# Kernel optimization log

Hardware: AMD Instinct MI355X
Metric: run time of the kernel (lower is better)

Reference implementation:

```python
import jax, jax.numpy as jnp
import numpy as np

B, CIN, N = 4, 128, 4096
CKEY, COUT = 64, 128

def setup_inputs() -> dict:
    key = jax.random.key(0)
    k1, k2, k3, k4 = jax.random.split(key, 4)
    x = jax.random.normal(k1, (B, CIN, N), dtype=jnp.float32)
    # Conv1d(kernel_size=1, bias=False) weights as [out, in] matrices
    Wq = jax.random.normal(k2, (CKEY, CIN), dtype=jnp.float32) * (1.0 / np.sqrt(CIN))
    Wk = jax.random.normal(k3, (CKEY, CIN), dtype=jnp.float32) * (1.0 / np.sqrt(CIN))
    Wv = jax.random.normal(k4, (COUT, CIN), dtype=jnp.float32) * (1.0 / np.sqrt(CIN))
    return {"x": x, "Wq": Wq, "Wk": Wk, "Wv": Wv}

def reference(x, Wq, Wk, Wv):
    # 1x1 conv projections: [B, C, N] -> [B, C', N]
    Q = jnp.einsum('ki,bin->bkn', Wq, x)   # [B, CKEY, N]
    K = jnp.einsum('ki,bin->bkn', Wk, x)   # [B, CKEY, N]
    V = jnp.einsum('oi,bin->bon', Wv, x)   # [B, COUT, N]
    # A = softmax(Q^T K) over last dim -- NOTE: no 1/sqrt(d) scaling, as in original
    scores = jnp.einsum('bkn,bkm->bnm', Q, K)     # [B, N, N]
    A = jax.nn.softmax(scores, axis=2)
    # out = (A @ V^T)^T -> [B, COUT, N]
    out = jnp.einsum('bnm,bom->bon', A, V)
    return out
```

## Files before the change

### kernel.cpp

```cpp
#include <hip/hip_runtime.h>
#include <hip/hip_bf16.h>

#define NN    4096
#define BB    4
#define CIN_  128
#define CKEY_ 64
#define COUT_ 128

typedef __attribute__((ext_vector_type(8))) short bf16x8;
typedef __attribute__((ext_vector_type(4))) short bf16x4;
typedef __attribute__((ext_vector_type(4))) float f32x4;

#define MFMA16 __builtin_amdgcn_mfma_f32_16x16x32_bf16
#define SWK(row, c) ((((row) << 6)) + ((((c) ^ ((row) & 7))) << 3))

__device__ __forceinline__ float bf2f(short s) {
    union { unsigned int u; float f; } c; c.u = ((unsigned int)(unsigned short)s) << 16; return c.f;
}
__device__ __forceinline__ short f2bf(float f) {
    union { float f; unsigned int u; } c; c.f = f;
    unsigned int r = c.u + 0x7fffu + ((c.u >> 16) & 1u);
    return (short)(r >> 16);
}
__device__ __forceinline__ float fexp2(float x) {
#if __has_builtin(__builtin_amdgcn_exp2f)
    return __builtin_amdgcn_exp2f(x);
#else
    return exp2f(x);
#endif
}
__device__ __forceinline__ unsigned int pack_bf16(float a, float b) {
    union { float f; unsigned int u; } ca, cb; ca.f = a; cb.f = b;
    unsigned int ua = ca.u + 0x8000u, ub = cb.u + 0x8000u;
#if __has_builtin(__builtin_amdgcn_perm)
    return __builtin_amdgcn_perm(ub, ua, 0x07060302u);
#else
    return (ua >> 16) | (ub & 0xffff0000u);
#endif
}

__global__ __launch_bounds__(256) void wcvt_kernel(const float* __restrict__ Wq,
                                                   const float* __restrict__ Wk,
                                                   const float* __restrict__ Wv,
                                                   short* __restrict__ Whf,
                                                   short* __restrict__ Wlf) {
    int id   = blockIdx.x * 256 + threadIdx.x;
    int l15  = id & 15;
    int quad = (id >> 4) & 3;
    int kc   = (id >> 6) & 3;
    int g    = id >> 8;
    int out  = g * 16 + l15;
    int k0   = kc * 32 + quad * 8;

    const float* src;
    float scale = 1.0f;
    if (out < 64)       { src = Wq + out * CIN_;         scale = 1.4426950408889634f; }
    else if (out < 128) { src = Wk + (out - 64) * CIN_; }
    else                { src = Wv + (out - 128) * CIN_; }

    bf16x8 h8, l8;
#pragma unroll
    for (int j = 0; j < 8; ++j) {
        float w = src[k0 + j] * scale;
        short h = f2bf(w);
        h8[j] = h;
        l8[j] = f2bf(w - bf2f(h));
    }
    *(bf16x8*)(Whf + id * 8) = h8;
    *(bf16x8*)(Wlf + id * 8) = l8;
}

__global__ __launch_bounds__(256) void proj_kernel(const float* __restrict__ x,
                                                   const short* __restrict__ Whf,
                                                   const short* __restrict__ Wlf,
                                                   short* __restrict__ Qh, short* __restrict__ Ql,
                                                   short* __restrict__ Kh, short* __restrict__ Kl,
                                                   short* __restrict__ Vb) {
    __shared__ __align__(16) short xsh[16 * 64 * 8];
    __shared__ __align__(16) short xsl[16 * 64 * 8];

    int tid  = threadIdx.x;
    int b    = blockIdx.y;
    int gz   = blockIdx.z;
    int gn0  = blockIdx.x * 64;
    int wave = tid >> 6;
    int lane = tid & 63;
    int quad = lane >> 4;
    int l15  = lane & 15;

    const float* xb = x + (size_t)b * CIN_ * NN + gn0;
#pragma unroll
    for (int rep = 0; rep < 4; ++rep) {
        int slot = rep * 256 + tid;
        int c = slot >> 6, n = slot & 63;
        bf16x8 h8, l8;
#pragma unroll
        for (int j = 0; j < 8; ++j) {
            float f = xb[(c * 8 + j) * NN + n];
            short h = f2bf(f);
            h8[j] = h;
            l8[j] = f2bf(f - bf2f(h));
        }
        *(bf16x8*)(xsh + (c * 64 + n) * 8) = h8;
        *(bf16x8*)(xsl + (c * 64 + n) * 8) = l8;
    }
    __syncthreads();

#pragma unroll
    for (int rr = 0; rr < 2; ++rr) {
        int rg = gz * 8 + rr * 4 + wave;
        f32x4 acc[4];
#pragma unroll
        for (int ct = 0; ct < 4; ++ct) acc[ct] = (f32x4){0.f, 0.f, 0.f, 0.f};

#pragma unroll
        for (int kc = 0; kc < 4; ++kc) {
            bf16x8 wh = *(const bf16x8*)(Whf + ((((rg * 4 + kc) * 4 + quad) * 16) + l15) * 8);
            bf16x8 wl = *(const bf16x8*)(Wlf + ((((rg * 4 + kc) * 4 + quad) * 16) + l15) * 8);
#pragma unroll
            for (int ct = 0; ct < 4; ++ct) {
                bf16x8 xh = *(const bf16x8*)(xsh + (((kc * 4 + quad) * 64) + ct * 16 + l15) * 8);
                bf16x8 xl = *(const bf16x8*)(xsl + (((kc * 4 + quad) * 64) + ct * 16 + l15) * 8);
                acc[ct] = MFMA16(wh, xh, acc[ct], 0, 0, 0);
                acc[ct] = MFMA16(wh, xl, acc[ct], 0, 0, 0);
                acc[ct] = MFMA16(wl, xh, acc[ct], 0, 0, 0);
            }
        }

        if (rg < 8) {
            short* H = (rg < 4) ? Qh : Kh;
            short* L = (rg < 4) ? Ql : Kl;
            int rb    = (rg < 4) ? rg : (rg - 4);
            int chunk = rb * 2 + (quad >> 1);
            int sub   = (quad & 1) * 4;
#pragma unroll
            for (int ct = 0; ct < 4; ++ct) {
                int n = gn0 + ct * 16 + l15;
                bf16x4 h4, l4;
#pragma unroll
                for (int r = 0; r < 4; ++r) {
                    float f = acc[ct][r];
                    short h = f2bf(f);
                    h4[r] = h;
                    l4[r] = f2bf(f - bf2f(h));
                }
                *(bf16x4*)(H + (((b * 8 + chunk) * NN) + n) * 8 + sub) = h4;
                *(bf16x4*)(L + (((b * 8 + chunk) * NN) + n) * 8 + sub) = l4;
            }
        } else {
            int o0 = rg * 16 + quad * 4 - 128;
#pragma unroll
            for (int ct = 0; ct < 4; ++ct) {
                int n = gn0 + ct * 16 + l15;
#pragma unroll
                for (int r = 0; r < 4; ++r)
                    Vb[((size_t)(b * COUT_ + o0 + r)) * NN + n] = f2bf(acc[ct][r]);
            }
        }
    }
}

__global__ __launch_bounds__(256, 2) void flash_kernel(const short* __restrict__ Qh,
                                                       const short* __restrict__ Ql,
                                                       const short* __restrict__ Kh,
                                                       const short* __restrict__ Kl,
                                                       const short* __restrict__ Vb,
                                                       float* __restrict__ outp,
                                                       float* __restrict__ ml,
                                                       int S, int direct) {
    __shared__ __align__(16) short KhT[64 * 64];
    __shared__ __align__(16) short KlT[64 * 64];
    __shared__ __align__(16) short VT[128 * 64];

    int tid  = threadIdx.x;
    int bx   = blockIdx.x;
    int b    = bx / S;
    int s    = bx - b * S;
    int qt   = blockIdx.y;
    int wave = tid >> 6;
    int lane = tid & 63;
    int quad = lane >> 4;
    int l15  = lane & 15;

    int nq0 = qt * 128 + wave * 32 + l15;
    bf16x8 qh0[2], qh1[2], ql0[2], ql1[2];
#pragma unroll
    for (int u = 0; u < 2; ++u) {
        int nq = nq0 + u * 16;
        qh0[u] = *(const bf16x8*)(Qh + (((b * 8 + quad)     * NN) + nq) * 8);
        qh1[u] = *(const bf16x8*)(Qh + (((b * 8 + 4 + quad) * NN) + nq) * 8);
        ql0[u] = *(const bf16x8*)(Ql + (((b * 8 + quad)     * NN) + nq) * 8);
        ql1[u] = *(const bf16x8*)(Ql + (((b * 8 + 4 + quad) * NN) + nq) * 8);
    }

    f32x4 O[2][8];
#pragma unroll
    for (int u = 0; u < 2; ++u)
#pragma unroll
        for (int f = 0; f < 8; ++f) O[u][f] = (f32x4){0.f, 0.f, 0.f, 0.f};
    float m_i[2] = {-1.0e30f, -1.0e30f}, l_i[2] = {0.f, 0.f};

    int krow = tid & 63, kc2 = (tid >> 6) * 2;
    int vrow = tid & 127, vc0 = (tid >> 7) * 4;
    int sl0 = (quad & 1) * 32 + l15;
    int sl1 = sl0 + 16;
    int fsel = quad >> 1;

    int KPS   = NN / S;
    int kb    = s * KPS;
    int iters = KPS / 64;

    const short* KhB = Kh + (size_t)b * 8 * NN * 8;
    const short* KlB = Kl + (size_t)b * 8 * NN * 8;
    const short* VbB = Vb + (size_t)b * COUT_ * NN;

    bf16x8 nkh[2], nkl[2], nv[4];
#pragma unroll
    for (int cc = 0; cc < 2; ++cc) {
        int c = kc2 + cc;
        nkh[cc] = *(const bf16x8*)(KhB + ((c * NN) + kb + krow) * 8);
        nkl[cc] = *(const bf16x8*)(KlB + ((c * NN) + kb + krow) * 8);
    }
#pragma unroll
    for (int q = 0; q < 4; ++q)
        nv[q] = *(const bf16x8*)(VbB + (size_t)vrow * NN + kb + (vc0 + q) * 8);

    for (int it = 0; it < iters; ++it) {
#pragma unroll
        for (int cc = 0; cc < 2; ++cc) {
            int c = kc2 + cc;
            *(bf16x8*)(KhT + SWK(krow, c)) = nkh[cc];
            *(bf16x8*)(KlT + SWK(krow, c)) = nkl[cc];
        }
#pragma unroll
        for (int q = 0; q < 4; ++q)
            *(bf16x8*)(VT + SWK(vrow, vc0 + q)) = nv[q];
        __syncthreads();

        if (it + 1 < iters) {
            int nb = kb + 64;
#pragma unroll
            for (int cc = 0; cc < 2; ++cc) {
                int c = kc2 + cc;
                nkh[cc] = *(const bf16x8*)(KhB + ((c * NN) + nb + krow) * 8);
                nkl[cc] = *(const bf16x8*)(KlB + ((c * NN) + nb + krow) * 8);
            }
#pragma unroll
            for (int q = 0; q < 4; ++q)
                nv[q] = *(const bf16x8*)(VbB + (size_t)vrow * NN + nb + (vc0 + q) * 8);
        }

        f32x4 sA[2][4];
#pragma unroll
        for (int f = 0; f < 4; ++f) {
            int row = f * 16 + l15;
            bf16x8 kh0 = *(const bf16x8*)(KhT + SWK(row, quad));
            bf16x8 kh1 = *(const bf16x8*)(KhT + SWK(row, 4 + quad));
            bf16x8 kl0 = *(const bf16x8*)(KlT + SWK(row, quad));
            bf16x8 kl1 = *(const bf16x8*)(KlT + SWK(row, 4 + quad));
#pragma unroll
            for (int u = 0; u < 2; ++u) {
                f32x4 acc = (f32x4){0.f, 0.f, 0.f, 0.f};
                acc = MFMA16(kh0, qh0[u], acc, 0, 0, 0);
                acc = MFMA16(kh1, qh1[u], acc, 0, 0, 0);
                acc = MFMA16(kl0, qh0[u], acc, 0, 0, 0);
                acc = MFMA16(kl1, qh1[u], acc, 0, 0, 0);
                acc = MFMA16(kh0, ql0[u], acc, 0, 0, 0);
                acc = MFMA16(kh1, ql1[u], acc, 0, 0, 0);
                sA[u][f] = acc;
            }
        }

        unsigned int pw[2][4][2];
#pragma unroll
        for (int u = 0; u < 2; ++u) {
            float vm = sA[u][0][0];
#pragma unroll
            for (int f = 0; f < 4; ++f)
#pragma unroll
                for (int r = 0; r < 4; ++r) vm = fmaxf(vm, sA[u][f][r]);
            vm = fmaxf(vm, __shfl_xor(vm, 16, 64));
            vm = fmaxf(vm, __shfl_xor(vm, 32, 64));
            float nm    = fmaxf(m_i[u], vm);
            float alpha = fexp2(m_i[u] - nm);
            m_i[u] = nm;

            float p[4][4];
            float rs = 0.f;
#pragma unroll
            for (int f = 0; f < 4; ++f)
#pragma unroll
                for (int r = 0; r < 4; ++r) {
                    float pv = fexp2(sA[u][f][r] - nm);
                    p[f][r] = pv;
                    rs += pv;
                }
            rs += __shfl_xor(rs, 16, 64);
            rs += __shfl_xor(rs, 32, 64);
            l_i[u] = l_i[u] * alpha + rs;

            if (__any(alpha < 1.0f)) {
#pragma unroll
                for (int f = 0; f < 8; ++f)
#pragma unroll
                    for (int r = 0; r < 4; ++r) O[u][f][r] *= alpha;
            }
#pragma unroll
            for (int f = 0; f < 4; ++f) {
                pw[u][f][0] = pack_bf16(p[f][0], p[f][1]);
                pw[u][f][1] = pack_bf16(p[f][2], p[f][3]);
            }
        }

#pragma unroll
        for (int g = 0; g < 2; ++g) {
            union { int i[4]; bf16x8 v; } pb[2];
#pragma unroll
            for (int u = 0; u < 2; ++u) {
                int a0 = __shfl((int)pw[u][g * 2][0],     sl0, 64);
                int a1 = __shfl((int)pw[u][g * 2][1],     sl0, 64);
                int a2 = __shfl((int)pw[u][g * 2][0],     sl1, 64);
                int a3 = __shfl((int)pw[u][g * 2][1],     sl1, 64);
                int b0 = __shfl((int)pw[u][g * 2 + 1][0], sl0, 64);
                int b1 = __shfl((int)pw[u][g * 2 + 1][1], sl0, 64);
                int b2 = __shfl((int)pw[u][g * 2 + 1][0], sl1, 64);
                int b3 = __shfl((int)pw[u][g * 2 + 1][1], sl1, 64);
                pb[u].i[0] = fsel ? b0 : a0;
                pb[u].i[1] = fsel ? b1 : a1;
                pb[u].i[2] = fsel ? b2 : a2;
                pb[u].i[3] = fsel ? b3 : a3;
            }
#pragma unroll
            for (int f8 = 0; f8 < 8; ++f8) {
                bf16x8 vA = *(const bf16x8*)(VT + SWK(f8 * 16 + l15, g * 4 + quad));
                O[0][f8] = MFMA16(vA, pb[0].v, O[0][f8], 0, 0, 0);
                O[1][f8] = MFMA16(vA, pb[1].v, O[1][f8], 0, 0, 0);
            }
        }
        __syncthreads();
        kb += 64;
    }

#pragma unroll
    for (int u = 0; u < 2; ++u) {
        int n = nq0 + u * 16;
        if (direct) {
            float inv = 1.f / l_i[u];
#pragma unroll
            for (int f8 = 0; f8 < 8; ++f8)
#pragma unroll
                for (int r = 0; r < 4; ++r) {
                    int o = f8 * 16 + quad * 4 + r;
                    outp[((size_t)(b * COUT_ + o)) * NN + n] = O[u][f8][r] * inv;
                }
        } else {
#pragma unroll
            for (int f8 = 0; f8 < 8; ++f8)
#pragma unroll
                for (int r = 0; r < 4; ++r) {
                    int o = f8 * 16 + quad * 4 + r;
                    outp[((size_t)((b * S + s) * COUT_ + o)) * NN + n] = O[u][f8][r];
                }
            if (quad == 0) {
                ml[((b * S + s) * 2 + 0) * NN + n] = m_i[u];
                ml[((b * S + s) * 2 + 1) * NN + n] = l_i[u];
            }
        }
    }
}

__global__ __launch_bounds__(256, 4) void merge_kernel(const float* __restrict__ Opart,
                                                       const float* __restrict__ ml,
                                                       float* __restrict__ out, int S) {
    int idx = blockIdx.x * 256 + threadIdx.x;
    int n0  = (idx & (NN / 4 - 1)) * 4;
    int rest = idx >> 10;
    int o = rest & (COUT_ - 1);
    int b = rest >> 7;

    f32x4 gm = (f32x4){-1.0e30f, -1.0e30f, -1.0e30f, -1.0e30f};
    for (int s = 0; s < S; ++s) {
        f32x4 m = *(const f32x4*)(ml + ((b * S + s) * 2 + 0) * NN + n0);
#pragma unroll
        for (int j = 0; j < 4; ++j) gm[j] = fmaxf(gm[j], m[j]);
    }
    f32x4 acc = (f32x4){0.f, 0.f, 0.f, 0.f};
    f32x4 den = (f32x4){0.f, 0.f, 0.f, 0.f};
    for (int s = 0; s < S; ++s) {
        f32x4 m = *(const f32x4*)(ml + ((b * S + s) * 2 + 0) * NN + n0);
        f32x4 l = *(const f32x4*)(ml + ((b * S + s) * 2 + 1) * NN + n0);
        f32x4 ov = *(const f32x4*)(Opart + ((size_t)((b * S + s) * COUT_ + o)) * NN + n0);
#pragma unroll
        for (int j = 0; j < 4; ++j) {
            float ws = fexp2(m[j] - gm[j]);
            acc[j] = fmaf(ws, ov[j], acc[j]);
            den[j] = fmaf(ws, l[j], den[j]);
        }
    }
    f32x4 res;
#pragma unroll
    for (int j = 0; j < 4; ++j) res[j] = acc[j] / den[j];
    *(f32x4*)(out + ((size_t)(b * COUT_ + o)) * NN + n0) = res;
}

extern "C" void kernel_launch(void* const* d_in, const int* in_sizes, int n_in,
                              void* d_out, int out_size, void* d_ws, size_t ws_size,
                              hipStream_t stream) {
    const float* x  = (const float*)d_in[0];
    const float* Wq = (const float*)d_in[1];
    const float* Wk = (const float*)d_in[2];
    const float* Wv = (const float*)d_in[3];

    char* ws = (char*)d_ws;
    short* Whf = (short*)ws;
    short* Wlf = (short*)(ws + 65536);
    short* Qh = (short*)(ws + 131072);
    short* Ql = Qh + 1048576;
    short* Kh = Ql + 1048576;
    short* Kl = Kh + 1048576;
    short* Vb = Kl + 1048576;
    size_t base = 131072 + 4ull * 2097152 + 4194304;
    const size_t OPART = 8388608;
    const size_t MLSZ  = 131072;

    int S;
    if      (ws_size >= base + 8 * (OPART + MLSZ)) S = 8;
    else if (ws_size >= base + 4 * (OPART + MLSZ)) S = 4;
    else if (ws_size >= base + 2 * (OPART + MLSZ)) S = 2;
    else                                           S = 1;
    int direct = (S == 1);

    float* mlp   = (float*)(ws + base);
    float* Opart = (float*)(ws + base + (size_t)S * MLSZ);

    wcvt_kernel<<<16, 256, 0, stream>>>(Wq, Wk, Wv, Whf, Wlf);
    proj_kernel<<<dim3(NN / 64, BB, 2), 256, 0, stream>>>(x, Whf, Wlf, Qh, Ql, Kh, Kl, Vb);
    flash_kernel<<<dim3(BB * S, NN / 128), 256, 0, stream>>>(
        Qh, Ql, Kh, Kl, Vb, direct ? (float*)d_out : Opart, mlp, S, direct);
    if (!direct)
        merge_kernel<<<BB * COUT_ * NN / 4 / 256, 256, 0, stream>>>(Opart, mlp, (float*)d_out, S);
}
```

Baseline: 146.6 us.

## Load K fragments directly from global memory and cap key split at four

K high/low fragments are now read from global memory straight into MFMA operand registers at the top of each iteration, instead of being staged through swizzled shared memory. This removes the KhT/KlT LDS buffers and their writes and reads, leaving only V in shared memory. The K loads are no longer prefetched one iteration ahead, so their latency can stall the first MFMAs. The maximum key-split factor also drops from 8 to 4, which halves the partial output traffic and merge work but gives fewer blocks and longer loops per block.

```diff
diff --git a/kernel.cpp b/kernel.cpp
--- a/kernel.cpp
+++ b/kernel.cpp
@@ -168,8 +168,6 @@
                                                        float* __restrict__ outp,
                                                        float* __restrict__ ml,
                                                        int S, int direct) {
-    __shared__ __align__(16) short KhT[64 * 64];
-    __shared__ __align__(16) short KlT[64 * 64];
     __shared__ __align__(16) short VT[128 * 64];
 
     int tid  = threadIdx.x;
@@ -200,7 +198,6 @@
         for (int f = 0; f < 8; ++f) O[u][f] = (f32x4){0.f, 0.f, 0.f, 0.f};
     float m_i[2] = {-1.0e30f, -1.0e30f}, l_i[2] = {0.f, 0.f};
 
-    int krow = tid & 63, kc2 = (tid >> 6) * 2;
     int vrow = tid & 127, vc0 = (tid >> 7) * 4;
     int sl0 = (quad & 1) * 32 + l15;
     int sl1 = sl0 + 16;
@@ -214,24 +211,22 @@
     const short* KlB = Kl + (size_t)b * 8 * NN * 8;
     const short* VbB = Vb + (size_t)b * COUT_ * NN;
 
-    bf16x8 nkh[2], nkl[2], nv[4];
-#pragma unroll
-    for (int cc = 0; cc < 2; ++cc) {
-        int c = kc2 + cc;
-        nkh[cc] = *(const bf16x8*)(KhB + ((c * NN) + kb + krow) * 8);
-        nkl[cc] = *(const bf16x8*)(KlB + ((c * NN) + kb + krow) * 8);
-    }
+    bf16x8 nv[4];
 #pragma unroll
     for (int q = 0; q < 4; ++q)
         nv[q] = *(const bf16x8*)(VbB + (size_t)vrow * NN + kb + (vc0 + q) * 8);
 
     for (int it = 0; it < iters; ++it) {
-#pragma unroll
-        for (int cc = 0; cc < 2; ++cc) {
-            int c = kc2 + cc;
-            *(bf16x8*)(KhT + SWK(krow, c)) = nkh[cc];
-            *(bf16x8*)(KlT + SWK(krow, c)) = nkl[cc];
-        }
+        bf16x8 kh0[4], kh1[4], kl0[4], kl1[4];
+#pragma unroll
+        for (int f = 0; f < 4; ++f) {
+            int row = kb + f * 16 + l15;
+            kh0[f] = *(const bf16x8*)(KhB + ((quad       * NN) + row) * 8);
+            kh1[f] = *(const bf16x8*)(KhB + (((4 + quad) * NN) + row) * 8);
+            kl0[f] = *(const bf16x8*)(KlB + ((quad       * NN) + row) * 8);
+            kl1[f] = *(const bf16x8*)(KlB + (((4 + quad) * NN) + row) * 8);
+        }
+
 #pragma unroll
         for (int q = 0; q < 4; ++q)
             *(bf16x8*)(VT + SWK(vrow, vc0 + q)) = nv[q];
@@ -240,12 +235,6 @@
         if (it + 1 < iters) {
             int nb = kb + 64;
 #pragma unroll
-            for (int cc = 0; cc < 2; ++cc) {
-                int c = kc2 + cc;
-                nkh[cc] = *(const bf16x8*)(KhB + ((c * NN) + nb + krow) * 8);
-                nkl[cc] = *(const bf16x8*)(KlB + ((c * NN) + nb + krow) * 8);
-            }
-#pragma unroll
             for (int q = 0; q < 4; ++q)
                 nv[q] = *(const bf16x8*)(VbB + (size_t)vrow * NN + nb + (vc0 + q) * 8);
         }
@@ -253,20 +242,15 @@
         f32x4 sA[2][4];
 #pragma unroll
         for (int f = 0; f < 4; ++f) {
-            int row = f * 16 + l15;
-            bf16x8 kh0 = *(const bf16x8*)(KhT + SWK(row, quad));
-            bf16x8 kh1 = *(const bf16x8*)(KhT + SWK(row, 4 + quad));
-            bf16x8 kl0 = *(const bf16x8*)(KlT + SWK(row, quad));
-            bf16x8 kl1 = *(const bf16x8*)(KlT + SWK(row, 4 + quad));
 #pragma unroll
             for (int u = 0; u < 2; ++u) {
                 f32x4 acc = (f32x4){0.f, 0.f, 0.f, 0.f};
-                acc = MFMA16(kh0, qh0[u], acc, 0, 0, 0);
-                acc = MFMA16(kh1, qh1[u], acc, 0, 0, 0);
-                acc = MFMA16(kl0, qh0[u], acc, 0, 0, 0);
-                acc = MFMA16(kl1, qh1[u], acc, 0, 0, 0);
-                acc = MFMA16(kh0, ql0[u], acc, 0, 0, 0);
-                acc = MFMA16(kh1, ql1[u], acc, 0, 0, 0);
+                acc = MFMA16(kh0[f], qh0[u], acc, 0, 0, 0);
+                acc = MFMA16(kh1[f], qh1[u], acc, 0, 0, 0);
+                acc = MFMA16(kl0[f], qh0[u], acc, 0, 0, 0);
+                acc = MFMA16(kl1[f], qh1[u], acc, 0, 0, 0);
+                acc = MFMA16(kh0[f], ql0[u], acc, 0, 0, 0);
+                acc = MFMA16(kh1[f], ql1[u], acc, 0, 0, 0);
                 sA[u][f] = acc;
             }
         }
@@ -424,8 +408,7 @@
     const size_t MLSZ  = 131072;
 
     int S;
-    if      (ws_size >= base + 8 * (OPART + MLSZ)) S = 8;
-    else if (ws_size >= base + 4 * (OPART + MLSZ)) S = 4;
+    if      (ws_size >= base + 4 * (OPART + MLSZ)) S = 4;
     else if (ws_size >= base + 2 * (OPART + MLSZ)) S = 2;
     else                                           S = 1;
     int direct = (S == 1);
```

Measured after the change: 136.5 us. 1.07x faster.
